# Kernel optimization log

Measured on AMD Instinct MI355X. Metric: run time of the kernel, lower is better.

Reference implementation:

```python
import jax, jax.numpy as jnp
import numpy as np

HIDDEN = 4096
N_HEADS = 32
HEAD_DIM = HIDDEN // N_HEADS
MAX_POS = 2048
ROPE_BASE = 10000.0


def _rope_tables(head_dim, max_pos):
    inv_freq = 1.0 / (ROPE_BASE ** (np.arange(0, head_dim, 2, dtype=np.float32) / head_dim))
    t = np.arange(max_pos, dtype=np.float32)
    freqs = np.einsum('i,j->ij', t, inv_freq)          # [max_pos, head_dim//2]
    emb = np.concatenate([freqs, freqs], axis=-1)       # [max_pos, head_dim]
    return jnp.asarray(np.cos(emb)), jnp.asarray(np.sin(emb))


def _rotate_half(x):
    x1, x2 = jnp.split(x, 2, axis=-1)
    return jnp.concatenate([-x2, x1], axis=-1)


def setup_inputs() -> dict:
    key = jax.random.key(0)
    ks = jax.random.split(key, 5)
    B, S = 1, 2048
    hidden_states = jax.random.normal(ks[0], (B, S, HIDDEN), dtype=jnp.float32)
    # additive causal mask (0 on/below diagonal, large negative above)
    causal = jnp.triu(jnp.full((S, S), -1e9, dtype=jnp.float32), k=1)
    attention_mask = causal[None, None, :, :]
    scale = 0.02
    wq = jax.random.normal(ks[1], (HIDDEN, HIDDEN), dtype=jnp.float32) * scale
    wk = jax.random.normal(ks[2], (HIDDEN, HIDDEN), dtype=jnp.float32) * scale
    wv = jax.random.normal(ks[3], (HIDDEN, HIDDEN), dtype=jnp.float32) * scale
    wo = jax.random.normal(ks[4], (HIDDEN, HIDDEN), dtype=jnp.float32) * scale
    position_ids = jnp.arange(S, dtype=jnp.int64 if jax.config.jax_enable_x64 else jnp.int32)[None, :]
    return {"hidden_states": hidden_states, "attention_mask": attention_mask,
            "wq": wq, "wk": wk, "wv": wv, "wo": wo, "position_ids": position_ids}


def reference(hidden_states, attention_mask, wq, wk, wv, wo, position_ids):
    B, S, H = hidden_states.shape
    cos_tab, sin_tab = _rope_tables(HEAD_DIM, MAX_POS)

    def shape_heads(x):  # [B,S,H] -> [B,nH,S,hd]
        return x.reshape(B, S, N_HEADS, HEAD_DIM).transpose(0, 2, 1, 3)

    # QKV projections (torch Linear: x @ W.T, no bias)
    q = shape_heads(hidden_states @ wq.T)
    k = shape_heads(hidden_states @ wk.T)
    v = shape_heads(hidden_states @ wv.T)

    # RoPE
    cos = cos_tab[position_ids][:, None, :, :]  # [B,1,S,hd]
    sin = sin_tab[position_ids][:, None, :, :]
    q = q * cos + _rotate_half(q) * sin
    k = k * cos + _rotate_half(k) * sin

    # scaled dot-product attention
    scale = 1.0 / jnp.sqrt(jnp.float32(HEAD_DIM))
    scores = jnp.einsum('bhqd,bhkd->bhqk', q, k) * scale
    scores = scores + attention_mask  # broadcast over heads
    scores = jnp.maximum(scores, jnp.finfo(scores.dtype).min)
    probs = jax.nn.softmax(scores, axis=-1)
    attn = jnp.einsum('bhqk,bhkd->bhqd', probs, v)

    # merge heads, output projection
    attn = attn.transpose(0, 2, 1, 3).reshape(B, S, H)
    return attn @ wo.T
```

## Files before the change

### kernel.cpp

```cpp
#include <hip/hip_runtime.h>

typedef __bf16 bf16x8 __attribute__((ext_vector_type(8)));
typedef float f32x4 __attribute__((ext_vector_type(4)));

__device__ __forceinline__ ushort f2bf(float f) {
  uint u = __builtin_bit_cast(uint, f);
  u = (u + 0x7fffu + ((u >> 16) & 1u)) >> 16;
  return (ushort)u;
}
__device__ __forceinline__ ushort f2bf_fast(float f) {
  uint u = __builtin_bit_cast(uint, f);
  return (ushort)((u + 0x8000u) >> 16);
}
__device__ __forceinline__ float bf2f(ushort h) {
  uint u = ((uint)h) << 16;
  return __builtin_bit_cast(float, u);
}
__device__ __forceinline__ float ex2(float x) {
  return __builtin_amdgcn_exp2f(x);
}

__device__ __forceinline__ void gload16(const ushort* g, ushort* l) {
  __builtin_amdgcn_global_load_lds(
      (const __attribute__((address_space(1))) unsigned int*)(const void*)g,
      (__attribute__((address_space(3))) unsigned int*)(void*)l, 16, 0, 0);
}

__global__ void cvt_f32_bf16_k(const float* __restrict__ in, ushort* __restrict__ out, int n4) {
  int i = blockIdx.x * blockDim.x + threadIdx.x;
  if (i >= n4) return;
  float4 v = reinterpret_cast<const float4*>(in)[i];
  ushort4 o;
  o.x = f2bf(v.x); o.y = f2bf(v.y); o.z = f2bf(v.z); o.w = f2bf(v.w);
  reinterpret_cast<ushort4*>(out)[i] = o;
}

__global__ void rope_tables_k(float* __restrict__ cosT, float* __restrict__ sinT) {
  int i = blockIdx.x * 256 + threadIdx.x;
  int p = i >> 6, j = i & 63;
  float inv = powf(10000.0f, -(float)j / 64.0f);
  float ang = (float)p * inv;
  cosT[i] = cosf(ang);
  sinT[i] = sinf(ang);
}

__global__ void rope_k(ushort* __restrict__ Q, ushort* __restrict__ K,
                       const float* __restrict__ cosT, const float* __restrict__ sinT,
                       const int* __restrict__ pos) {
  int idx = blockIdx.x * 256 + threadIdx.x;
  int s = idx >> 11;
  int rest = idx & 2047;
  int h = rest >> 6, d = rest & 63;
  int p = pos[s];
  float c = cosT[p * 64 + d], sn = sinT[p * 64 + d];
  size_t base = (size_t)s * 4096 + h * 128 + d;
  float q1 = bf2f(Q[base]), q2 = bf2f(Q[base + 64]);
  Q[base]      = f2bf(q1 * c - q2 * sn);
  Q[base + 64] = f2bf(q2 * c + q1 * sn);
  float k1 = bf2f(K[base]), k2 = bf2f(K[base + 64]);
  K[base]      = f2bf(k1 * c - k2 * sn);
  K[base + 64] = f2bf(k2 * c + k1 * sn);
}

template<typename TA, typename TW, int OMODE>
__global__ __launch_bounds__(256) void gemm_bt(const TA* __restrict__ A, const TW* __restrict__ W,
                                               void* __restrict__ Cout) {
  constexpr int K = 4096, N = 4096;
  constexpr bool BF = (sizeof(TA) == 2);
  __shared__ ushort As[128 * 64];
  __shared__ ushort Ws[128 * 64];
  const int tid = threadIdx.x;
  const int w = tid >> 6, lane = tid & 63, g = lane >> 4, r = lane & 15;
  const int wr = w >> 1, wc = w & 1;
  const int id = blockIdx.x;
  const int xcd = id & 7, slot = id >> 3;
  const int nb = (xcd & 3) * 8 + (slot & 7);
  const int mb = (xcd >> 2) * 8 + (slot >> 3);
  const int m0 = mb * 128, n0 = nb * 128;

  f32x4 acc[4][4];
#pragma unroll
  for (int i = 0; i < 4; i++)
#pragma unroll
    for (int j = 0; j < 4; j++) acc[i][j] = f32x4{0.f, 0.f, 0.f, 0.f};

  for (int k0 = 0; k0 < K; k0 += 64) {
    if (k0) __syncthreads();
    if constexpr (BF) {
#pragma unroll
      for (int i = 0; i < 4; i++) {
        int r0 = (w * 4 + i) * 8;
        int row = r0 + (lane >> 3), c = lane & 7;
        int cs = (c ^ (row & 7)) * 8;
        gload16((const ushort*)A + (size_t)(m0 + row) * K + k0 + cs, &As[r0 * 64]);
        gload16((const ushort*)W + (size_t)(n0 + row) * K + k0 + cs, &Ws[r0 * 64]);
      }
    } else {
#pragma unroll
      for (int i = 0; i < 4; i++) {
        int li = tid + i * 256, row = li >> 3, c = li & 7;
        int cs = (c ^ (row & 7)) * 8;
        float4 v0 = *reinterpret_cast<const float4*>(A + (size_t)(m0 + row) * K + k0 + cs);
        float4 v1 = *reinterpret_cast<const float4*>(A + (size_t)(m0 + row) * K + k0 + cs + 4);
        ushort o[8] = {f2bf(v0.x), f2bf(v0.y), f2bf(v0.z), f2bf(v0.w),
                       f2bf(v1.x), f2bf(v1.y), f2bf(v1.z), f2bf(v1.w)};
        *reinterpret_cast<uint4*>(&As[row * 64 + c * 8]) = *reinterpret_cast<uint4*>(o);
      }
#pragma unroll
      for (int i = 0; i < 4; i++) {
        int li = tid + i * 256, row = li >> 3, c = li & 7;
        int cs = (c ^ (row & 7)) * 8;
        float4 v0 = *reinterpret_cast<const float4*>(W + (size_t)(n0 + row) * K + k0 + cs);
        float4 v1 = *reinterpret_cast<const float4*>(W + (size_t)(n0 + row) * K + k0 + cs + 4);
        ushort o[8] = {f2bf(v0.x), f2bf(v0.y), f2bf(v0.z), f2bf(v0.w),
                       f2bf(v1.x), f2bf(v1.y), f2bf(v1.z), f2bf(v1.w)};
        *reinterpret_cast<uint4*>(&Ws[row * 64 + c * 8]) = *reinterpret_cast<uint4*>(o);
      }
    }
    __syncthreads();

#pragma unroll
    for (int kk = 0; kk < 2; kk++) {
      bf16x8 af[4], bfr[4];
#pragma unroll
      for (int mi = 0; mi < 4; mi++) {
        int row = wr * 64 + mi * 16 + r;
        af[mi] = *reinterpret_cast<const bf16x8*>((const char*)As + row * 128 + (((g + kk * 4) ^ (r & 7)) * 16));
      }
#pragma unroll
      for (int nj = 0; nj < 4; nj++) {
        int row = wc * 64 + nj * 16 + r;
        bfr[nj] = *reinterpret_cast<const bf16x8*>((const char*)Ws + row * 128 + (((g + kk * 4) ^ (r & 7)) * 16));
      }
#pragma unroll
      for (int mi = 0; mi < 4; mi++)
#pragma unroll
        for (int nj = 0; nj < 4; nj++)
          acc[mi][nj] = __builtin_amdgcn_mfma_f32_16x16x32_bf16(af[mi], bfr[nj], acc[mi][nj], 0, 0, 0);
    }
  }

  if constexpr (OMODE == 0) {
    float* C = (float*)Cout;
#pragma unroll
    for (int mi = 0; mi < 4; mi++)
#pragma unroll
      for (int nj = 0; nj < 4; nj++)
#pragma unroll
        for (int j = 0; j < 4; j++) {
          int row = m0 + wr * 64 + mi * 16 + g * 4 + j;
          int col = n0 + wc * 64 + nj * 16 + r;
          C[(size_t)row * N + col] = acc[mi][nj][j];
        }
  } else if constexpr (OMODE == 1) {
    ushort* C = (ushort*)Cout;
#pragma unroll
    for (int mi = 0; mi < 4; mi++)
#pragma unroll
      for (int nj = 0; nj < 4; nj++)
#pragma unroll
        for (int j = 0; j < 4; j++) {
          int row = m0 + wr * 64 + mi * 16 + g * 4 + j;
          int col = n0 + wc * 64 + nj * 16 + r;
          C[(size_t)row * N + col] = f2bf(acc[mi][nj][j]);
        }
  } else {
    ushort* C = (ushort*)Cout;
#pragma unroll
    for (int mi = 0; mi < 4; mi++)
#pragma unroll
      for (int nj = 0; nj < 4; nj++) {
        int col = n0 + wc * 64 + nj * 16 + r;
        int row0 = m0 + wr * 64 + mi * 16 + g * 4;
        ushort4 v;
        v.x = f2bf(acc[mi][nj][0]); v.y = f2bf(acc[mi][nj][1]);
        v.z = f2bf(acc[mi][nj][2]); v.w = f2bf(acc[mi][nj][3]);
        *reinterpret_cast<ushort4*>(C + (size_t)col * 2048 + row0) = v;
      }
  }
}

__global__ __launch_bounds__(256) void attn_fwd(const ushort* __restrict__ Q, const ushort* __restrict__ K,
                                                const ushort* __restrict__ Vt, ushort* __restrict__ O) {
  constexpr int S = 2048, HD = 4096;
  constexpr float SC2 = 0.12753102f;
  constexpr float THR = 90.50967f;
  __shared__ ushort Ks[2][64 * 128];
  __shared__ ushort Vs[2][128 * 64];
  __shared__ ushort Ps[4][16 * 64];
  const int id = blockIdx.x;
  const int xcd = id & 7, slot = id >> 3;
  const int h = xcd * 4 + (slot & 3);
  const int qx = slot >> 2;
  const int tid = threadIdx.x;
  const int w = tid >> 6, lane = tid & 63, g = lane >> 4, r = lane & 15;
  const int kRow = lane >> 4, kC = lane & 15;
  const int vRow = lane >> 3, vC = lane & 7;

#pragma unroll 1
  for (int pass = 0; pass < 2; ++pass) {
    const int qtile = pass ? (31 - qx) : qx;
    const int qbase = qtile * 64;
    const int nt = qtile + 1;

    bf16x8 qf[4];
    {
      const int qrow = qbase + w * 16 + r;
#pragma unroll
      for (int dc = 0; dc < 4; dc++)
        qf[dc] = *reinterpret_cast<const bf16x8*>(Q + (size_t)qrow * HD + h * 128 + dc * 32 + g * 8);
    }

    f32x4 o[8];
#pragma unroll
    for (int i = 0; i < 8; i++) o[i] = f32x4{0.f, 0.f, 0.f, 0.f};
    float m[4] = {-3e38f, -3e38f, -3e38f, -3e38f};
    float l[4] = {0.f, 0.f, 0.f, 0.f};

    __syncthreads();
#pragma unroll
    for (int i = 0; i < 4; i++) {
      int kr0 = (w * 4 + i) * 4, krow = kr0 + kRow;
      gload16(K + (size_t)krow * HD + h * 128 + (kC ^ (krow & 7)) * 8, &Ks[0][kr0 * 128]);
      int vr0 = (w * 4 + i) * 8, vrow = vr0 + vRow;
      gload16(Vt + (size_t)(h * 128 + vrow) * S + (vC ^ (vrow & 7)) * 8, &Vs[0][vr0 * 64]);
    }

#pragma unroll 1
    for (int t = 0; t < nt; ++t) {
      const int kv0 = t * 64;
      const int buf = t & 1;
      __syncthreads();
      if (t + 1 < nt) {
        const int kvn = kv0 + 64;
#pragma unroll
        for (int i = 0; i < 4; i++) {
          int kr0 = (w * 4 + i) * 4, krow = kr0 + kRow;
          gload16(K + (size_t)(kvn + krow) * HD + h * 128 + (kC ^ (krow & 7)) * 8, &Ks[buf ^ 1][kr0 * 128]);
          int vr0 = (w * 4 + i) * 8, vrow = vr0 + vRow;
          gload16(Vt + (size_t)(h * 128 + vrow) * S + kvn + (vC ^ (vrow & 7)) * 8, &Vs[buf ^ 1][vr0 * 64]);
        }
      }

      f32x4 sc[4];
      __builtin_amdgcn_s_setprio(1);
#pragma unroll
      for (int c = 0; c < 4; c++) {
        f32x4 tacc = f32x4{0.f, 0.f, 0.f, 0.f};
        const int krow = c * 16 + r;
        const char* kb = (const char*)&Ks[buf][0] + krow * 256;
#pragma unroll
        for (int dc = 0; dc < 4; dc++) {
          bf16x8 kf = *reinterpret_cast<const bf16x8*>(kb + ((dc * 64 + g * 16) ^ ((krow & 7) << 4)));
          tacc = __builtin_amdgcn_mfma_f32_16x16x32_bf16(qf[dc], kf, tacc, 0, 0, 0);
        }
        sc[c] = tacc;
      }
      __builtin_amdgcn_s_setprio(0);

      if (t == nt - 1) {
#pragma unroll
        for (int c = 0; c < 4; c++) {
          int kvg = kv0 + c * 16 + r;
#pragma unroll
          for (int j = 0; j < 4; j++) {
            int qg = qbase + w * 16 + g * 4 + j;
            if (kvg > qg) sc[c][j] = -3e38f;
          }
        }
      }

      float pm[4];
#pragma unroll
      for (int j = 0; j < 4; j++)
        pm[j] = fmaxf(fmaxf(sc[0][j], sc[1][j]), fmaxf(sc[2][j], sc[3][j]));
#pragma unroll
      for (int st = 1; st < 16; st <<= 1) {
        float t0 = __shfl_xor(pm[0], st);
        float t1 = __shfl_xor(pm[1], st);
        float t2 = __shfl_xor(pm[2], st);
        float t3 = __shfl_xor(pm[3], st);
        pm[0] = fmaxf(pm[0], t0); pm[1] = fmaxf(pm[1], t1);
        pm[2] = fmaxf(pm[2], t2); pm[3] = fmaxf(pm[3], t3);
      }

      bool ok = (pm[0] - m[0] <= THR) && (pm[1] - m[1] <= THR) &&
                (pm[2] - m[2] <= THR) && (pm[3] - m[3] <= THR);
      if (!__all(ok)) {
#pragma unroll
        for (int j = 0; j < 4; j++) {
          float mn = fmaxf(m[j], pm[j]);
          float alpha = ex2((m[j] - mn) * SC2);
          m[j] = mn;
          l[j] *= alpha;
#pragma unroll
          for (int dc = 0; dc < 8; dc++) o[dc][j] *= alpha;
        }
      }

      float ps[4];
      char* pb = (char*)&Ps[w][0];
#pragma unroll
      for (int j = 0; j < 4; j++) {
        float mb = m[j] * SC2;
        float p0 = ex2(__builtin_fmaf(sc[0][j], SC2, -mb));
        float p1 = ex2(__builtin_fmaf(sc[1][j], SC2, -mb));
        float p2 = ex2(__builtin_fmaf(sc[2][j], SC2, -mb));
        float p3 = ex2(__builtin_fmaf(sc[3][j], SC2, -mb));
        ps[j] = (p0 + p1) + (p2 + p3);
        int ql = g * 4 + j;
        char* pr = pb + (size_t)ql * 128;
        uint sw = (ql & 7) << 4;
        *reinterpret_cast<ushort*>(pr + ((0 * 32 + r * 2) ^ sw)) = f2bf_fast(p0);
        *reinterpret_cast<ushort*>(pr + ((1 * 32 + r * 2) ^ sw)) = f2bf_fast(p1);
        *reinterpret_cast<ushort*>(pr + ((2 * 32 + r * 2) ^ sw)) = f2bf_fast(p2);
        *reinterpret_cast<ushort*>(pr + ((3 * 32 + r * 2) ^ sw)) = f2bf_fast(p3);
      }
#pragma unroll
      for (int st = 1; st < 16; st <<= 1) {
        float t0 = __shfl_xor(ps[0], st);
        float t1 = __shfl_xor(ps[1], st);
        float t2 = __shfl_xor(ps[2], st);
        float t3 = __shfl_xor(ps[3], st);
        ps[0] += t0; ps[1] += t1; ps[2] += t2; ps[3] += t3;
      }
#pragma unroll
      for (int j = 0; j < 4; j++) l[j] += ps[j];

      __builtin_amdgcn_s_setprio(1);
#pragma unroll
      for (int c2 = 0; c2 < 2; c2++) {
        bf16x8 pf = *reinterpret_cast<const bf16x8*>(pb + (size_t)r * 128 + ((c2 * 64 + g * 16) ^ ((r & 7) << 4)));
#pragma unroll
        for (int dc = 0; dc < 8; dc++) {
          const int vrow = dc * 16 + r;
          bf16x8 vf = *reinterpret_cast<const bf16x8*>((const char*)&Vs[buf][0] + vrow * 128 + ((c2 * 64 + g * 16) ^ ((vrow & 7) << 4)));
          o[dc] = __builtin_amdgcn_mfma_f32_16x16x32_bf16(pf, vf, o[dc], 0, 0, 0);
        }
      }
      __builtin_amdgcn_s_setprio(0);
    }

#pragma unroll
    for (int dc = 0; dc < 8; dc++)
#pragma unroll
      for (int j = 0; j < 4; j++) {
        float v = o[dc][j] / l[j];
        O[(size_t)(qbase + w * 16 + g * 4 + j) * HD + h * 128 + dc * 16 + r] = f2bf(v);
      }
  }
}

extern "C" void kernel_launch(void* const* d_in, const int* in_sizes, int n_in,
                              void* d_out, int out_size, void* d_ws, size_t ws_size,
                              hipStream_t stream) {
  const float* X  = (const float*)d_in[0];
  const float* Wq = (const float*)d_in[2];
  const float* Wk = (const float*)d_in[3];
  const float* Wv = (const float*)d_in[4];
  const float* Wo = (const float*)d_in[5];
  const int* pos  = (const int*)d_in[6];
  float* out = (float*)d_out;
  char* ws = (char*)d_ws;
  const size_t MB = 1024ull * 1024ull;

  float*  tabC = (float*)(ws + 0);
  float*  tabS = (float*)(ws + 512 * 1024);
  ushort* Qb   = (ushort*)(ws + 1 * MB);
  ushort* Kb   = (ushort*)(ws + 17 * MB);
  ushort* Vt   = (ushort*)(ws + 33 * MB);
  ushort* Ab   = (ushort*)(ws + 49 * MB);
  ushort* Xb   = (ushort*)(ws + 65 * MB);
  ushort* Wb   = (ushort*)(ws + 81 * MB);
  const bool fast = ws_size >= 113 * MB;

  rope_tables_k<<<512, 256, 0, stream>>>(tabC, tabS);

  if (fast) {
    cvt_f32_bf16_k<<<8192, 256, 0, stream>>>(X, Xb, 2097152);
    cvt_f32_bf16_k<<<16384, 256, 0, stream>>>(Wq, Wb, 4194304);
    gemm_bt<ushort, ushort, 1><<<512, 256, 0, stream>>>(Xb, Wb, Qb);
    cvt_f32_bf16_k<<<16384, 256, 0, stream>>>(Wk, Wb, 4194304);
    gemm_bt<ushort, ushort, 1><<<512, 256, 0, stream>>>(Xb, Wb, Kb);
    cvt_f32_bf16_k<<<16384, 256, 0, stream>>>(Wv, Wb, 4194304);
    gemm_bt<ushort, ushort, 2><<<512, 256, 0, stream>>>(Xb, Wb, Vt);
    rope_k<<<16384, 256, 0, stream>>>(Qb, Kb, tabC, tabS, pos);
    attn_fwd<<<512, 256, 0, stream>>>(Qb, Kb, Vt, Ab);
    cvt_f32_bf16_k<<<16384, 256, 0, stream>>>(Wo, Wb, 4194304);
    gemm_bt<ushort, ushort, 0><<<512, 256, 0, stream>>>(Ab, Wb, out);
  } else {
    gemm_bt<float, float, 1><<<512, 256, 0, stream>>>(X, Wq, Qb);
    gemm_bt<float, float, 1><<<512, 256, 0, stream>>>(X, Wk, Kb);
    gemm_bt<float, float, 2><<<512, 256, 0, stream>>>(X, Wv, Vt);
    rope_k<<<16384, 256, 0, stream>>>(Qb, Kb, tabC, tabS, pos);
    attn_fwd<<<512, 256, 0, stream>>>(Qb, Kb, Vt, Ab);
    gemm_bt<ushort, float, 0><<<512, 256, 0, stream>>>(Ab, Wo, out);
  }
}
```

Before: 470.9 us.

## Fuse fp32 weight conversion into GEMM loads and reorder attention PV MFMA

Drops the separate fp32-to-bf16 weight conversion kernels and lets each GEMM read fp32 weights directly, converting them to bf16 while staging into shared memory. This removes a full read/write pass over each weight matrix and lowers the workspace requirement. The weight loads become synchronous, twice as wide, and repeated across M-blocks, which may slow the GEMM main loop. In attention, the P·V MFMAs are issued before the row-sum shuffle reduction to overlap the two, and the final normalization uses a reciprocal multiply instead of division.

After: 558.9 us. 18.7% more time.

```diff
diff --git a/kernel.cpp b/kernel.cpp
--- a/kernel.cpp
+++ b/kernel.cpp
@@ -66,7 +66,6 @@
 __global__ __launch_bounds__(256) void gemm_bt(const TA* __restrict__ A, const TW* __restrict__ W,
                                                void* __restrict__ Cout) {
   constexpr int K = 4096, N = 4096;
-  constexpr bool BF = (sizeof(TA) == 2);
   __shared__ ushort As[128 * 64];
   __shared__ ushort Ws[128 * 64];
   const int tid = threadIdx.x;
@@ -86,32 +85,43 @@
 
   for (int k0 = 0; k0 < K; k0 += 64) {
     if (k0) __syncthreads();
-    if constexpr (BF) {
+    if constexpr (sizeof(TA) == 2) {
 #pragma unroll
       for (int i = 0; i < 4; i++) {
         int r0 = (w * 4 + i) * 8;
         int row = r0 + (lane >> 3), c = lane & 7;
         int cs = (c ^ (row & 7)) * 8;
         gload16((const ushort*)A + (size_t)(m0 + row) * K + k0 + cs, &As[r0 * 64]);
-        gload16((const ushort*)W + (size_t)(n0 + row) * K + k0 + cs, &Ws[r0 * 64]);
       }
     } else {
 #pragma unroll
       for (int i = 0; i < 4; i++) {
         int li = tid + i * 256, row = li >> 3, c = li & 7;
         int cs = (c ^ (row & 7)) * 8;
-        float4 v0 = *reinterpret_cast<const float4*>(A + (size_t)(m0 + row) * K + k0 + cs);
-        float4 v1 = *reinterpret_cast<const float4*>(A + (size_t)(m0 + row) * K + k0 + cs + 4);
+        const float* src = (const float*)A + (size_t)(m0 + row) * K + k0 + cs;
+        float4 v0 = *reinterpret_cast<const float4*>(src);
+        float4 v1 = *reinterpret_cast<const float4*>(src + 4);
         ushort o[8] = {f2bf(v0.x), f2bf(v0.y), f2bf(v0.z), f2bf(v0.w),
                        f2bf(v1.x), f2bf(v1.y), f2bf(v1.z), f2bf(v1.w)};
         *reinterpret_cast<uint4*>(&As[row * 64 + c * 8]) = *reinterpret_cast<uint4*>(o);
       }
+    }
+    if constexpr (sizeof(TW) == 2) {
+#pragma unroll
+      for (int i = 0; i < 4; i++) {
+        int r0 = (w * 4 + i) * 8;
+        int row = r0 + (lane >> 3), c = lane & 7;
+        int cs = (c ^ (row & 7)) * 8;
+        gload16((const ushort*)W + (size_t)(n0 + row) * K + k0 + cs, &Ws[r0 * 64]);
+      }
+    } else {
 #pragma unroll
       for (int i = 0; i < 4; i++) {
         int li = tid + i * 256, row = li >> 3, c = li & 7;
         int cs = (c ^ (row & 7)) * 8;
-        float4 v0 = *reinterpret_cast<const float4*>(W + (size_t)(n0 + row) * K + k0 + cs);
-        float4 v1 = *reinterpret_cast<const float4*>(W + (size_t)(n0 + row) * K + k0 + cs + 4);
+        const float* src = (const float*)W + (size_t)(n0 + row) * K + k0 + cs;
+        float4 v0 = *reinterpret_cast<const float4*>(src);
+        float4 v1 = *reinterpret_cast<const float4*>(src + 4);
         ushort o[8] = {f2bf(v0.x), f2bf(v0.y), f2bf(v0.z), f2bf(v0.w),
                        f2bf(v1.x), f2bf(v1.y), f2bf(v1.z), f2bf(v1.w)};
         *reinterpret_cast<uint4*>(&Ws[row * 64 + c * 8]) = *reinterpret_cast<uint4*>(o);
@@ -316,6 +326,20 @@
         *reinterpret_cast<ushort*>(pr + ((2 * 32 + r * 2) ^ sw)) = f2bf_fast(p2);
         *reinterpret_cast<ushort*>(pr + ((3 * 32 + r * 2) ^ sw)) = f2bf_fast(p3);
       }
+
+      __builtin_amdgcn_s_setprio(1);
+#pragma unroll
+      for (int c2 = 0; c2 < 2; c2++) {
+        bf16x8 pf = *reinterpret_cast<const bf16x8*>(pb + (size_t)r * 128 + ((c2 * 64 + g * 16) ^ ((r & 7) << 4)));
+#pragma unroll
+        for (int dc = 0; dc < 8; dc++) {
+          const int vrow = dc * 16 + r;
+          bf16x8 vf = *reinterpret_cast<const bf16x8*>((const char*)&Vs[buf][0] + vrow * 128 + ((c2 * 64 + g * 16) ^ ((vrow & 7) << 4)));
+          o[dc] = __builtin_amdgcn_mfma_f32_16x16x32_bf16(pf, vf, o[dc], 0, 0, 0);
+        }
+      }
+      __builtin_amdgcn_s_setprio(0);
+
 #pragma unroll
       for (int st = 1; st < 16; st <<= 1) {
         float t0 = __shfl_xor(ps[0], st);
@@ -326,26 +350,16 @@
       }
 #pragma unroll
       for (int j = 0; j < 4; j++) l[j] += ps[j];
-
-      __builtin_amdgcn_s_setprio(1);
-#pragma unroll
-      for (int c2 = 0; c2 < 2; c2++) {
-        bf16x8 pf = *reinterpret_cast<const bf16x8*>(pb + (size_t)r * 128 + ((c2 * 64 + g * 16) ^ ((r & 7) << 4)));
-#pragma unroll
-        for (int dc = 0; dc < 8; dc++) {
-          const int vrow = dc * 16 + r;
-          bf16x8 vf = *reinterpret_cast<const bf16x8*>((const char*)&Vs[buf][0] + vrow * 128 + ((c2 * 64 + g * 16) ^ ((vrow & 7) << 4)));
-          o[dc] = __builtin_amdgcn_mfma_f32_16x16x32_bf16(pf, vf, o[dc], 0, 0, 0);
-        }
-      }
-      __builtin_amdgcn_s_setprio(0);
-    }
-
+    }
+
+    float rl[4];
+#pragma unroll
+    for (int j = 0; j < 4; j++) rl[j] = __builtin_amdgcn_rcpf(l[j]);
 #pragma unroll
     for (int dc = 0; dc < 8; dc++)
 #pragma unroll
       for (int j = 0; j < 4; j++) {
-        float v = o[dc][j] / l[j];
+        float v = o[dc][j] * rl[j];
         O[(size_t)(qbase + w * 16 + g * 4 + j) * HD + h * 128 + dc * 16 + r] = f2bf(v);
       }
   }
@@ -371,23 +385,18 @@
   ushort* Vt   = (ushort*)(ws + 33 * MB);
   ushort* Ab   = (ushort*)(ws + 49 * MB);
   ushort* Xb   = (ushort*)(ws + 65 * MB);
-  ushort* Wb   = (ushort*)(ws + 81 * MB);
-  const bool fast = ws_size >= 113 * MB;
+  const bool fast = ws_size >= 82 * MB;
 
   rope_tables_k<<<512, 256, 0, stream>>>(tabC, tabS);
 
   if (fast) {
     cvt_f32_bf16_k<<<8192, 256, 0, stream>>>(X, Xb, 2097152);
-    cvt_f32_bf16_k<<<16384, 256, 0, stream>>>(Wq, Wb, 4194304);
-    gemm_bt<ushort, ushort, 1><<<512, 256, 0, stream>>>(Xb, Wb, Qb);
-    cvt_f32_bf16_k<<<16384, 256, 0, stream>>>(Wk, Wb, 4194304);
-    gemm_bt<ushort, ushort, 1><<<512, 256, 0, stream>>>(Xb, Wb, Kb);
-    cvt_f32_bf16_k<<<16384, 256, 0, stream>>>(Wv, Wb, 4194304);
-    gemm_bt<ushort, ushort, 2><<<512, 256, 0, stream>>>(Xb, Wb, Vt);
+    gemm_bt<ushort, float, 1><<<512, 256, 0, stream>>>(Xb, Wq, Qb);
+    gemm_bt<ushort, float, 1><<<512, 256, 0, stream>>>(Xb, Wk, Kb);
+    gemm_bt<ushort, float, 2><<<512, 256, 0, stream>>>(Xb, Wv, Vt);
     rope_k<<<16384, 256, 0, stream>>>(Qb, Kb, tabC, tabS, pos);
     attn_fwd<<<512, 256, 0, stream>>>(Qb, Kb, Vt, Ab);
-    cvt_f32_bf16_k<<<16384, 256, 0, stream>>>(Wo, Wb, 4194304);
-    gemm_bt<ushort, ushort, 0><<<512, 256, 0, stream>>>(Ab, Wb, out);
+    gemm_bt<ushort, float, 0><<<512, 256, 0, stream>>>(Ab, Wo, out);
   } else {
     gemm_bt<float, float, 1><<<512, 256, 0, stream>>>(X, Wq, Qb);
     gemm_bt<float, float, 1><<<512, 256, 0, stream>>>(X, Wk, Kb);
```

## Double-buffer GEMM LDS tiles and reorder attention PV MFMA before row-sum shuffles

Applied to the files above, without the earlier changes.

The GEMM now keeps two LDS buffers for the A and W tiles and issues the load for tile t+1 before computing on tile t, so there is one barrier per K step and global loads overlap the MFMAs. In the attention kernel the P·V MFMA block moves ahead of the cross-lane shuffle reduction of the row sums, so the shuffles can overlap matrix work. The final normalisation uses a hardware reciprocal multiply instead of a divide. Doubling LDS to 64 KB per GEMM block may lower occupancy, and the fp32-input path holds more registers in flight.

Measured after the change: 467.3 us. Within noise of the previous version (-0.8%).

```diff
diff --git a/kernel.cpp b/kernel.cpp
--- a/kernel.cpp
+++ b/kernel.cpp
@@ -65,10 +65,10 @@
 template<typename TA, typename TW, int OMODE>
 __global__ __launch_bounds__(256) void gemm_bt(const TA* __restrict__ A, const TW* __restrict__ W,
                                                void* __restrict__ Cout) {
-  constexpr int K = 4096, N = 4096;
-  constexpr bool BF = (sizeof(TA) == 2);
-  __shared__ ushort As[128 * 64];
-  __shared__ ushort Ws[128 * 64];
+  constexpr int K = 4096, N = 4096, NT = K / 64;
+  constexpr bool BF = (sizeof(TA) == 2 && sizeof(TW) == 2);
+  __shared__ ushort As[2][128 * 64];
+  __shared__ ushort Ws[2][128 * 64];
   const int tid = threadIdx.x;
   const int w = tid >> 6, lane = tid & 63, g = lane >> 4, r = lane & 15;
   const int wr = w >> 1, wc = w & 1;
@@ -78,59 +78,63 @@
   const int mb = (xcd >> 2) * 8 + (slot >> 3);
   const int m0 = mb * 128, n0 = nb * 128;
 
-  f32x4 acc[4][4];
-#pragma unroll
-  for (int i = 0; i < 4; i++)
-#pragma unroll
-    for (int j = 0; j < 4; j++) acc[i][j] = f32x4{0.f, 0.f, 0.f, 0.f};
-
-  for (int k0 = 0; k0 < K; k0 += 64) {
-    if (k0) __syncthreads();
+  auto stage = [&](int t, int b) {
+    const int k0 = t * 64;
     if constexpr (BF) {
 #pragma unroll
       for (int i = 0; i < 4; i++) {
         int r0 = (w * 4 + i) * 8;
         int row = r0 + (lane >> 3), c = lane & 7;
         int cs = (c ^ (row & 7)) * 8;
-        gload16((const ushort*)A + (size_t)(m0 + row) * K + k0 + cs, &As[r0 * 64]);
-        gload16((const ushort*)W + (size_t)(n0 + row) * K + k0 + cs, &Ws[r0 * 64]);
+        gload16((const ushort*)A + (size_t)(m0 + row) * K + k0 + cs, &As[b][r0 * 64]);
+        gload16((const ushort*)W + (size_t)(n0 + row) * K + k0 + cs, &Ws[b][r0 * 64]);
       }
     } else {
 #pragma unroll
       for (int i = 0; i < 4; i++) {
         int li = tid + i * 256, row = li >> 3, c = li & 7;
         int cs = (c ^ (row & 7)) * 8;
-        float4 v0 = *reinterpret_cast<const float4*>(A + (size_t)(m0 + row) * K + k0 + cs);
-        float4 v1 = *reinterpret_cast<const float4*>(A + (size_t)(m0 + row) * K + k0 + cs + 4);
-        ushort o[8] = {f2bf(v0.x), f2bf(v0.y), f2bf(v0.z), f2bf(v0.w),
-                       f2bf(v1.x), f2bf(v1.y), f2bf(v1.z), f2bf(v1.w)};
-        *reinterpret_cast<uint4*>(&As[row * 64 + c * 8]) = *reinterpret_cast<uint4*>(o);
-      }
-#pragma unroll
-      for (int i = 0; i < 4; i++) {
-        int li = tid + i * 256, row = li >> 3, c = li & 7;
-        int cs = (c ^ (row & 7)) * 8;
-        float4 v0 = *reinterpret_cast<const float4*>(W + (size_t)(n0 + row) * K + k0 + cs);
-        float4 v1 = *reinterpret_cast<const float4*>(W + (size_t)(n0 + row) * K + k0 + cs + 4);
-        ushort o[8] = {f2bf(v0.x), f2bf(v0.y), f2bf(v0.z), f2bf(v0.w),
-                       f2bf(v1.x), f2bf(v1.y), f2bf(v1.z), f2bf(v1.w)};
-        *reinterpret_cast<uint4*>(&Ws[row * 64 + c * 8]) = *reinterpret_cast<uint4*>(o);
+        const float* srcA = (const float*)A + (size_t)(m0 + row) * K + k0 + cs;
+        float4 a0 = *reinterpret_cast<const float4*>(srcA);
+        float4 a1 = *reinterpret_cast<const float4*>(srcA + 4);
+        ushort oa[8] = {f2bf(a0.x), f2bf(a0.y), f2bf(a0.z), f2bf(a0.w),
+                        f2bf(a1.x), f2bf(a1.y), f2bf(a1.z), f2bf(a1.w)};
+        *reinterpret_cast<uint4*>(&As[b][row * 64 + c * 8]) = *reinterpret_cast<uint4*>(oa);
+        const float* srcW = (const float*)W + (size_t)(n0 + row) * K + k0 + cs;
+        float4 w0 = *reinterpret_cast<const float4*>(srcW);
+        float4 w1 = *reinterpret_cast<const float4*>(srcW + 4);
+        ushort ow[8] = {f2bf(w0.x), f2bf(w0.y), f2bf(w0.z), f2bf(w0.w),
+                        f2bf(w1.x), f2bf(w1.y), f2bf(w1.z), f2bf(w1.w)};
+        *reinterpret_cast<uint4*>(&Ws[b][row * 64 + c * 8]) = *reinterpret_cast<uint4*>(ow);
       }
     }
-    __syncthreads();
-
+  };
+
+  f32x4 acc[4][4];
+#pragma unroll
+  for (int i = 0; i < 4; i++)
+#pragma unroll
+    for (int j = 0; j < 4; j++) acc[i][j] = f32x4{0.f, 0.f, 0.f, 0.f};
+
+  stage(0, 0);
+  __syncthreads();
+
+#pragma unroll 1
+  for (int t = 0; t < NT; ++t) {
+    const int buf = t & 1;
+    if (t + 1 < NT) stage(t + 1, buf ^ 1);
 #pragma unroll
     for (int kk = 0; kk < 2; kk++) {
       bf16x8 af[4], bfr[4];
 #pragma unroll
       for (int mi = 0; mi < 4; mi++) {
         int row = wr * 64 + mi * 16 + r;
-        af[mi] = *reinterpret_cast<const bf16x8*>((const char*)As + row * 128 + (((g + kk * 4) ^ (r & 7)) * 16));
+        af[mi] = *reinterpret_cast<const bf16x8*>((const char*)&As[buf][0] + row * 128 + (((g + kk * 4) ^ (r & 7)) * 16));
       }
 #pragma unroll
       for (int nj = 0; nj < 4; nj++) {
         int row = wc * 64 + nj * 16 + r;
-        bfr[nj] = *reinterpret_cast<const bf16x8*>((const char*)Ws + row * 128 + (((g + kk * 4) ^ (r & 7)) * 16));
+        bfr[nj] = *reinterpret_cast<const bf16x8*>((const char*)&Ws[buf][0] + row * 128 + (((g + kk * 4) ^ (r & 7)) * 16));
       }
 #pragma unroll
       for (int mi = 0; mi < 4; mi++)
@@ -138,6 +142,7 @@
         for (int nj = 0; nj < 4; nj++)
           acc[mi][nj] = __builtin_amdgcn_mfma_f32_16x16x32_bf16(af[mi], bfr[nj], acc[mi][nj], 0, 0, 0);
     }
+    __syncthreads();
   }
 
   if constexpr (OMODE == 0) {
@@ -316,6 +321,20 @@
         *reinterpret_cast<ushort*>(pr + ((2 * 32 + r * 2) ^ sw)) = f2bf_fast(p2);
         *reinterpret_cast<ushort*>(pr + ((3 * 32 + r * 2) ^ sw)) = f2bf_fast(p3);
       }
+
+      __builtin_amdgcn_s_setprio(1);
+#pragma unroll
+      for (int c2 = 0; c2 < 2; c2++) {
+        bf16x8 pf = *reinterpret_cast<const bf16x8*>(pb + (size_t)r * 128 + ((c2 * 64 + g * 16) ^ ((r & 7) << 4)));
+#pragma unroll
+        for (int dc = 0; dc < 8; dc++) {
+          const int vrow = dc * 16 + r;
+          bf16x8 vf = *reinterpret_cast<const bf16x8*>((const char*)&Vs[buf][0] + vrow * 128 + ((c2 * 64 + g * 16) ^ ((vrow & 7) << 4)));
+          o[dc] = __builtin_amdgcn_mfma_f32_16x16x32_bf16(pf, vf, o[dc], 0, 0, 0);
+        }
+      }
+      __builtin_amdgcn_s_setprio(0);
+
 #pragma unroll
       for (int st = 1; st < 16; st <<= 1) {
         float t0 = __shfl_xor(ps[0], st);
@@ -326,26 +345,16 @@
       }
 #pragma unroll
       for (int j = 0; j < 4; j++) l[j] += ps[j];
-
-      __builtin_amdgcn_s_setprio(1);
-#pragma unroll
-      for (int c2 = 0; c2 < 2; c2++) {
-        bf16x8 pf = *reinterpret_cast<const bf16x8*>(pb + (size_t)r * 128 + ((c2 * 64 + g * 16) ^ ((r & 7) << 4)));
-#pragma unroll
-        for (int dc = 0; dc < 8; dc++) {
-          const int vrow = dc * 16 + r;
-          bf16x8 vf = *reinterpret_cast<const bf16x8*>((const char*)&Vs[buf][0] + vrow * 128 + ((c2 * 64 + g * 16) ^ ((vrow & 7) << 4)));
-          o[dc] = __builtin_amdgcn_mfma_f32_16x16x32_bf16(pf, vf, o[dc], 0, 0, 0);
-        }
-      }
-      __builtin_amdgcn_s_setprio(0);
     }
 
+    float rl[4];
+#pragma unroll
+    for (int j = 0; j < 4; j++) rl[j] = __builtin_amdgcn_rcpf(l[j]);
 #pragma unroll
     for (int dc = 0; dc < 8; dc++)
 #pragma unroll
       for (int j = 0; j < 4; j++) {
-        float v = o[dc][j] / l[j];
+        float v = o[dc][j] * rl[j];
         O[(size_t)(qbase + w * 16 + g * 4 + j) * HD + h * 128 + dc * 16 + r] = f2bf(v);
       }
   }
```
